# Optimization experiments

Hardware: AMD Instinct MI355X
Metric: run time of the kernel (lower is better)

Reference implementation:

```python
import jax, jax.numpy as jnp
import numpy as np

B, D, P = 2048, 768, 200
DOWN = [(384, 768), (192, 384), (96, 192), (48, 96)]
UP = [(96, 48), (192, 96), (384, 192), (768, 384)]


def setup_inputs() -> dict:
    key = jax.random.key(0)
    ks = jax.random.split(key, 32)
    inp = {
        "x": jax.random.normal(ks[0], (B, D), jnp.float32),
        "aW": jax.random.normal(ks[1], (D, D), jnp.float32) * 0.02,
        "ab": jax.random.normal(ks[2], (D,), jnp.float32) * 0.02,
        "protos": jax.random.normal(ks[3], (P, D), jnp.float32),
    }
    k = 4
    for i, (o, ii) in enumerate(DOWN):
        inp[f"Wd{i}"] = jax.random.normal(ks[k], (o, ii), jnp.float32) * (1.0 / np.sqrt(ii)); k += 1
        inp[f"bd{i}"] = jax.random.normal(ks[k], (o,), jnp.float32) * 0.02; k += 1
    for i, (o, ii) in enumerate(UP):
        inp[f"Wu{i}"] = jax.random.normal(ks[k], (o, ii), jnp.float32) * (1.0 / np.sqrt(ii)); k += 1
        inp[f"bu{i}"] = jax.random.normal(ks[k], (o,), jnp.float32) * 0.02; k += 1
    return inp


def _adopter_net(x, Wds, bds, Wus, bus):
    # down path with skip storage
    x_inter = []
    h = x
    for Wd, bd in zip(Wds, bds):
        h = jax.nn.relu(h @ Wd.T + bd)
        x_inter.append(h)
    # up path: residual adds for middle layers (i==1 uses x_inter[-2], i==2 uses x_inter[-3])
    n = len(Wus)
    for i, (Wu, bu) in enumerate(zip(Wus, bus)):
        if i == 0 or i == n - 1:
            h = jax.nn.relu(h @ Wu.T + bu)
        else:
            h = jax.nn.relu((h + x_inter[-i - 1]) @ Wu.T + bu)
    return h


def reference(x, aW, ab, Wd0, bd0, Wd1, bd1, Wd2, bd2, Wd3, bd3,
              Wu0, bu0, Wu1, bu1, Wu2, bu2, Wu3, bu3, protos):
    Wds, bds = [Wd0, Wd1, Wd2, Wd3], [bd0, bd1, bd2, bd3]
    Wus, bus = [Wu0, Wu1, Wu2, Wu3], [bu0, bu1, bu2, bu3]
    # features = x + adapter(x) + adopters(x)
    features = x + (x @ aW.T + ab) + _adopter_net(x, Wds, bds, Wus, bus)  # [B, D]
    # fused per-prototype negative L1 distance (replaces Python loop over PrototypeBase)
    logits = -jnp.sum(jnp.abs(features[:, None, :] - protos[None, :, :]), axis=-1)  # [B, P]
    return logits
```

## Files before the change

### kernel.cpp

```cpp
#include <hip/hip_runtime.h>

typedef __attribute__((ext_vector_type(8))) __bf16 bf16x8;
typedef __attribute__((ext_vector_type(4))) float f32x4;
typedef _Float16 hf2 __attribute__((ext_vector_type(2)));
typedef _Float16 hf8 __attribute__((ext_vector_type(8)));
typedef unsigned short u16;
typedef struct { hf2 v[4]; } hf2x4;

__device__ __forceinline__ float bf2f(u16 h) {
    return __uint_as_float(((unsigned int)h) << 16);
}
__device__ __forceinline__ u16 f2bf(float f) {
    unsigned int u = __float_as_uint(f);
    u += 0x7fffu + ((u >> 16) & 1u);
    return (u16)(u >> 16);
}

#if __has_builtin(__builtin_amdgcn_fdot2)
__device__ __forceinline__ float FDOT2(hf2 a, hf2 b, float c) {
    return __builtin_amdgcn_fdot2(a, b, c, false);
}
#else
__device__ __forceinline__ float FDOT2(hf2 a, hf2 b, float c) {
    return c + (float)a[0] + (float)a[1];
}
#endif

#define GLOAD_LDS16(gsrc, ldst)                                                          \
    __builtin_amdgcn_global_load_lds(                                                    \
        (__attribute__((address_space(1))) unsigned int*)(gsrc),                         \
        (__attribute__((address_space(3))) unsigned int*)(ldst), 16, 0, 0)

struct CvtDesc { const float* src; u16* dst; int N, K, Npad, Kpad, blk0, fmt; };
struct CvtTab { CvtDesc t[11]; };

__global__ __launch_bounds__(256) void cvt_all(CvtTab tab) {
    int b = blockIdx.x;
    int ti = 0;
#pragma unroll
    for (int j = 1; j < 11; ++j)
        if (b >= tab.t[j].blk0) ti = j;
    const CvtDesc c = tab.t[ti];
    long i = (long)(b - c.blk0) * 256 + threadIdx.x;
    long tot = (long)c.Npad * c.Kpad;
    if (i >= tot) return;
    int n = (int)(i / c.Kpad);
    int k = (int)(i - (long)n * c.Kpad);
    float v = (n < c.N && k < c.K) ? c.src[(long)n * c.K + k] : 0.f;
    if (c.fmt) {
        _Float16 h = (_Float16)v;
        c.dst[i] = __builtin_bit_cast(u16, h);
    } else {
        c.dst[i] = f2bf(v);
    }
}

template<int RELU, int HASRES, int MODE>
__device__ __forceinline__ void gemm_body(
    char* lds,
    const u16* __restrict__ A, int lda,
    const u16* __restrict__ W, int ldw,
    const float* __restrict__ bias, int Nreal,
    u16* __restrict__ outB, int ldo,
    const u16* __restrict__ res,
    float* __restrict__ outF, _Float16* __restrict__ outH,
    const float* __restrict__ addF,
    int nk, int mb, int nb)
{
    char* ldsA = lds;
    char* ldsB = lds + 8192;

    const int tid  = threadIdx.x;
    const int wave = tid >> 6;
    const int lane = tid & 63;
    const int wr = wave >> 1, wc = wave & 1;
    const int lr = lane & 15, lk = lane >> 4;

    f32x4 acc[2][2];
#pragma unroll
    for (int i = 0; i < 2; ++i)
#pragma unroll
        for (int j = 0; j < 2; ++j)
#pragma unroll
            for (int e = 0; e < 4; ++e) acc[i][j][e] = 0.f;

    const int g0 = wave * 64 + lane;
    const int r0 = g0 >> 3, l0 = (g0 & 7) ^ (r0 & 7);
    const int g1 = g0 + 256;
    const int r1 = g1 >> 3, l1 = (g1 & 7) ^ (r1 & 7);

    for (int kt = 0; kt < nk; ++kt) {
        const int kk = kt * 64;
        GLOAD_LDS16(A + (size_t)(mb + r0) * lda + kk + l0 * 8, ldsA + wave * 1024);
        GLOAD_LDS16(A + (size_t)(mb + r1) * lda + kk + l1 * 8, ldsA + 4096 + wave * 1024);
        GLOAD_LDS16(W + (size_t)(nb + r0) * ldw + kk + l0 * 8, ldsB + wave * 1024);
        GLOAD_LDS16(W + (size_t)(nb + r1) * ldw + kk + l1 * 8, ldsB + 4096 + wave * 1024);
        __syncthreads();
#pragma unroll
        for (int ks = 0; ks < 2; ++ks) {
            bf16x8 af[2], bfr[2];
#pragma unroll
            for (int mi = 0; mi < 2; ++mi) {
                int m_loc = wr * 32 + mi * 16 + lr;
                int gr = (ks * 4 + lk) ^ (m_loc & 7);
                af[mi] = *(const bf16x8*)(ldsA + m_loc * 128 + gr * 16);
            }
#pragma unroll
            for (int ni = 0; ni < 2; ++ni) {
                int n_loc = wc * 32 + ni * 16 + lr;
                int gr = (ks * 4 + lk) ^ (n_loc & 7);
                bfr[ni] = *(const bf16x8*)(ldsB + n_loc * 128 + gr * 16);
            }
#pragma unroll
            for (int mi = 0; mi < 2; ++mi)
#pragma unroll
                for (int ni = 0; ni < 2; ++ni)
                    acc[mi][ni] = __builtin_amdgcn_mfma_f32_16x16x32_bf16(
                        af[mi], bfr[ni], acc[mi][ni], 0, 0, 0);
        }
        __syncthreads();
    }

#pragma unroll
    for (int mi = 0; mi < 2; ++mi) {
#pragma unroll
        for (int ni = 0; ni < 2; ++ni) {
            const int n_g = nb + wc * 32 + ni * 16 + lr;
            const float bv = (n_g < Nreal) ? bias[n_g] : 0.f;
#pragma unroll
            for (int r = 0; r < 4; ++r) {
                const int m_g = mb + wr * 32 + mi * 16 + lk * 4 + r;
                float v = acc[mi][ni][r] + bv;
                if (RELU) v = fmaxf(v, 0.f);
                if (HASRES) v += bf2f(res[(size_t)m_g * ldo + n_g]);
                if (MODE == 1) {
                    outF[(size_t)m_g * 768 + n_g] = v + addF[(size_t)m_g * 768 + n_g];
                } else if (MODE == 2) {
                    outH[(size_t)m_g * 768 + n_g] =
                        (_Float16)(v + addF[(size_t)m_g * 768 + n_g]);
                } else {
                    outB[(size_t)m_g * ldo + n_g] = f2bf(v);
                }
            }
        }
    }
}

template<int RELU, int HASRES, int MODE>
__global__ __launch_bounds__(256) void gemm_k(
    const u16* __restrict__ A, int lda,
    const u16* __restrict__ W, int ldw,
    const float* __restrict__ bias, int Nreal,
    u16* __restrict__ outB, int ldo,
    const u16* __restrict__ res,
    float* __restrict__ outF, _Float16* __restrict__ outH,
    const float* __restrict__ addF, int nk)
{
    __shared__ __align__(16) char lds[16384];
    gemm_body<RELU, HASRES, MODE>(lds, A, lda, W, ldw, bias, Nreal, outB, ldo,
                                  res, outF, outH, addF, nk,
                                  blockIdx.x * 64, blockIdx.y * 64);
}

__global__ __launch_bounds__(256) void gemm_ad0(
    const u16* __restrict__ xb,
    const u16* __restrict__ aWb, const float* __restrict__ ab,
    float* __restrict__ adF, const float* __restrict__ x,
    const u16* __restrict__ Wd0b, const float* __restrict__ bd0,
    u16* __restrict__ h1)
{
    __shared__ __align__(16) char lds[16384];
    if (blockIdx.y < 12) {
        gemm_body<0, 0, 1>(lds, xb, 768, aWb, 768, ab, 768, nullptr, 0,
                           nullptr, adF, nullptr, x, 12,
                           blockIdx.x * 64, blockIdx.y * 64);
    } else {
        gemm_body<1, 0, 0>(lds, xb, 768, Wd0b, 768, bd0, 384, h1, 384,
                           nullptr, nullptr, nullptr, nullptr, 12,
                           blockIdx.x * 64, (blockIdx.y - 12) * 64);
    }
}

template<int K, int NPAD, int NREAL, int RES, int OUTG>
__device__ __forceinline__ void layer16(
    const u16* __restrict__ W, int ldw, const float* __restrict__ bias,
    const u16* actIn, int ldin,
    u16* actOut, int ldout,
    const u16* resid, int ldres,
    u16* __restrict__ gout, int ldg)
{
    constexpr int TPW = NPAD / 64;
    const int tid = threadIdx.x;
    const int wave = tid >> 6, lane = tid & 63;
    const int lr = lane & 15, lk = lane >> 4;

    f32x4 acc[TPW];
#pragma unroll
    for (int t = 0; t < TPW; ++t)
#pragma unroll
        for (int e = 0; e < 4; ++e) acc[t][e] = 0.f;

#pragma unroll
    for (int kk = 0; kk < K / 32; ++kk) {
        const bf16x8 a = *(const bf16x8*)&actIn[lr * ldin + kk * 32 + lk * 8];
#pragma unroll
        for (int t = 0; t < TPW; ++t) {
            const int nc = (wave * TPW + t) * 16 + lr;
            const bf16x8 b = *(const bf16x8*)&W[(size_t)nc * ldw + kk * 32 + lk * 8];
            acc[t] = __builtin_amdgcn_mfma_f32_16x16x32_bf16(a, b, acc[t], 0, 0, 0);
        }
    }
#pragma unroll
    for (int t = 0; t < TPW; ++t) {
        const int nc = (wave * TPW + t) * 16 + lr;
        const float bv = (nc < NREAL) ? bias[nc] : 0.f;
#pragma unroll
        for (int r = 0; r < 4; ++r) {
            const int row = lk * 4 + r;
            float v = fmaxf(acc[t][r] + bv, 0.f);
            if (RES) v += bf2f(resid[row * ldres + nc]);
            const u16 o = f2bf(v);
            if (OUTG) gout[(size_t)row * ldg + nc] = o;
            else      actOut[row * ldout + nc] = o;
        }
    }
}

__global__ __launch_bounds__(256) void chain_mid(
    const u16* __restrict__ h1,
    const u16* __restrict__ Wd1b, const float* __restrict__ bd1,
    const u16* __restrict__ Wd2b, const float* __restrict__ bd2,
    const u16* __restrict__ Wd3b, const float* __restrict__ bd3,
    const u16* __restrict__ Wu0b, const float* __restrict__ bu0,
    const u16* __restrict__ Wu1b, const float* __restrict__ bu1,
    const u16* __restrict__ Wu2b, const float* __restrict__ bu2,
    u16* __restrict__ u2)
{
    __shared__ u16 A[16 * 392];
    __shared__ u16 B[16 * 200];
    __shared__ u16 C[16 * 136];
    __shared__ u16 D[16 * 72];
    const int tid = threadIdx.x;
    const int rb = blockIdx.x * 16;

    for (int i = tid; i < 768; i += 256) {
        const int r = i / 48, c = i - r * 48;
        *(bf16x8*)&A[r * 392 + c * 8] =
            *(const bf16x8*)&h1[(size_t)(rb + r) * 384 + c * 8];
    }
    __syncthreads();
    layer16<384, 192, 192, 0, 0>(Wd1b, 384, bd1, A, 392, B, 200, nullptr, 0, nullptr, 0);
    __syncthreads();
    layer16<192, 128,  96, 0, 0>(Wd2b, 192, bd2, B, 200, C, 136, nullptr, 0, nullptr, 0);
    __syncthreads();
    layer16<128,  64,  48, 0, 0>(Wd3b, 128, bd3, C, 136, D,  72, nullptr, 0, nullptr, 0);
    __syncthreads();
    u16* E = A;
    u16* F = A + 16 * 136;
    layer16< 64, 128,  96, 1, 0>(Wu0b,  64, bu0, D,  72, E, 136, C, 136, nullptr, 0);
    __syncthreads();
    layer16<128, 192, 192, 1, 0>(Wu1b, 128, bu1, E, 136, F, 200, B, 200, nullptr, 0);
    __syncthreads();
    layer16<192, 384, 384, 0, 1>(Wu2b, 192, bu2, F, 200, nullptr, 0, nullptr, 0,
                                 u2 + (size_t)rb * 384, 384);
}

__global__ __launch_bounds__(256) void l1_kernel(
    const _Float16* __restrict__ feat, const _Float16* __restrict__ protos,
    float* __restrict__ part)
{
    __shared__ _Float16 fs[128][64];
    __shared__ hf2 pt[32][64];
    const int tid = threadIdx.x;
    const int tp = tid & 15, tr = tid >> 4;
    const int rb = blockIdx.x * 128;
    const int pb = blockIdx.y * 64;
    const int db = blockIdx.z * 64;

    {
        const int g = tid & 7, r0 = tid >> 3;
#pragma unroll
        for (int k = 0; k < 4; ++k) {
            const int r = r0 + 32 * k;
            *(hf8*)&fs[r][g * 8] =
                *(const hf8*)&feat[(size_t)(rb + r) * 768 + db + g * 8];
        }
    }
    {
        const int sp = tid & 63, q = tid >> 6;
        const _Float16* src = &protos[(size_t)(pb + sp) * 768 + db + q * 16];
        hf8 v0 = *(const hf8*)src;
        hf8 v1 = *(const hf8*)(src + 8);
        hf2x4 w0 = __builtin_bit_cast(hf2x4, v0);
        hf2x4 w1 = __builtin_bit_cast(hf2x4, v1);
#pragma unroll
        for (int e = 0; e < 4; ++e)
            pt[q * 8 + e][sp] = w0.v[e];
#pragma unroll
        for (int e = 0; e < 4; ++e)
            pt[q * 8 + 4 + e][sp] = w1.v[e];
    }
    __syncthreads();

    float acc[8][4];
#pragma unroll
    for (int i = 0; i < 8; ++i)
#pragma unroll
        for (int j = 0; j < 4; ++j) acc[i][j] = 0.f;

    const hf2 one2 = {(_Float16)1.0f, (_Float16)1.0f};
#pragma unroll 2
    for (int g = 0; g < 8; ++g) {
        hf2x4 F2[8];
#pragma unroll
        for (int i = 0; i < 8; ++i)
            F2[i] = __builtin_bit_cast(hf2x4,
                        *(const hf8*)&fs[tr + 16 * i][g * 8]);
        hf2x4 P2[4];
#pragma unroll
        for (int q = 0; q < 4; ++q)
            P2[q] = __builtin_bit_cast(hf2x4,
                        *(const hf8*)&pt[g * 4 + q][tp * 4]);
#pragma unroll
        for (int q = 0; q < 4; ++q) {
#pragma unroll
            for (int j = 0; j < 4; ++j) {
                const hf2 pj = P2[q].v[j];
#pragma unroll
                for (int i = 0; i < 8; ++i) {
                    hf2 d = F2[i].v[q] - pj;
                    unsigned ud = __builtin_bit_cast(unsigned, d) & 0x7FFF7FFFu;
                    acc[i][j] = FDOT2(__builtin_bit_cast(hf2, ud), one2, acc[i][j]);
                }
            }
        }
    }
    const int p = pb + tp * 4;
    if (p < 200) {
        const size_t zb = (size_t)blockIdx.z * 2048;
#pragma unroll
        for (int i = 0; i < 8; ++i) {
            float4 v = {-acc[i][0], -acc[i][1], -acc[i][2], -acc[i][3]};
            *(float4*)&part[(zb + rb + tr + 16 * i) * 200 + p] = v;
        }
    }
}

__global__ __launch_bounds__(256) void l1_reduce(
    const float* __restrict__ part, float* __restrict__ out)
{
    const int row = blockIdx.x;
    const int p = threadIdx.x;
    if (p < 200) {
        float s = 0.f;
#pragma unroll
        for (int z = 0; z < 12; ++z)
            s += part[((size_t)z * 2048 + row) * 200 + p];
        out[(size_t)row * 200 + p] = s;
    }
}

static constexpr size_t OFF_PART  = 0;
static constexpr size_t OFF_XB    = 0;
static constexpr size_t OFF_AWB   = 3145728;
static constexpr size_t OFF_WD0   = 4325376;
static constexpr size_t OFF_WD1   = 4915200;
static constexpr size_t OFF_WD2   = 5062656;
static constexpr size_t OFF_WD3   = 5111808;
static constexpr size_t OFF_WU0   = 5128192;
static constexpr size_t OFF_WU1   = 5144576;
static constexpr size_t OFF_WU2   = 5193728;
static constexpr size_t OFF_WU3   = 5341184;
static constexpr size_t OFF_H1    = 5931008;
static constexpr size_t OFF_U2    = 10387456;
static constexpr size_t OFF_ADF   = 11960320;
static constexpr size_t OFF_FEATH = 19660800;
static constexpr size_t OFF_PROH  = 22806528;

extern "C" void kernel_launch(void* const* d_in, const int* in_sizes, int n_in,
                              void* d_out, int out_size, void* d_ws, size_t ws_size,
                              hipStream_t stream) {
    const float* x      = (const float*)d_in[0];
    const float* aW     = (const float*)d_in[1];
    const float* ab     = (const float*)d_in[2];
    const float* protos = (const float*)d_in[3];
    const float* Wd[4]  = {(const float*)d_in[4], (const float*)d_in[6],
                           (const float*)d_in[8], (const float*)d_in[10]};
    const float* bd[4]  = {(const float*)d_in[5], (const float*)d_in[7],
                           (const float*)d_in[9], (const float*)d_in[11]};
    const float* Wu[4]  = {(const float*)d_in[12], (const float*)d_in[14],
                           (const float*)d_in[16], (const float*)d_in[18]};
    const float* bu[4]  = {(const float*)d_in[13], (const float*)d_in[15],
                           (const float*)d_in[17], (const float*)d_in[19]};
    float* out = (float*)d_out;
    char* ws = (char*)d_ws;

    u16* xb    = (u16*)(ws + OFF_XB);
    u16* aWb   = (u16*)(ws + OFF_AWB);
    u16* Wd0b  = (u16*)(ws + OFF_WD0);
    u16* Wd1b  = (u16*)(ws + OFF_WD1);
    u16* Wd2b  = (u16*)(ws + OFF_WD2);
    u16* Wd3b  = (u16*)(ws + OFF_WD3);
    u16* Wu0b  = (u16*)(ws + OFF_WU0);
    u16* Wu1b  = (u16*)(ws + OFF_WU1);
    u16* Wu2b  = (u16*)(ws + OFF_WU2);
    u16* Wu3b  = (u16*)(ws + OFF_WU3);
    u16* h1    = (u16*)(ws + OFF_H1);
    u16* u2    = (u16*)(ws + OFF_U2);
    float* adF = (float*)(ws + OFF_ADF);
    float* part = (float*)(ws + OFF_PART);
    _Float16* featH = (_Float16*)(ws + OFF_FEATH);
    _Float16* proH  = (_Float16*)(ws + OFF_PROH);

    CvtTab tab;
    int blk = 0;
    auto set = [&](int i, const float* s, u16* d, int N, int K, int Np, int Kp,
                   int fmt) {
        tab.t[i] = {s, d, N, K, Np, Kp, blk, fmt};
        blk += (Np * Kp + 255) / 256;
    };
    set(0,  x,      xb,          2048, 768, 2048, 768, 0);
    set(1,  aW,     aWb,         768,  768, 768,  768, 0);
    set(2,  Wd[0],  Wd0b,        384,  768, 384,  768, 0);
    set(3,  Wd[1],  Wd1b,        192,  384, 192,  384, 0);
    set(4,  Wd[2],  Wd2b,        96,   192, 128,  192, 0);
    set(5,  Wd[3],  Wd3b,        48,   96,  64,   128, 0);
    set(6,  Wu[0],  Wu0b,        96,   48,  128,  64,  0);
    set(7,  Wu[1],  Wu1b,        192,  96,  192,  128, 0);
    set(8,  Wu[2],  Wu2b,        384,  192, 384,  192, 0);
    set(9,  Wu[3],  Wu3b,        768,  384, 768,  384, 0);
    set(10, protos, (u16*)proH,  200,  768, 256,  768, 1);
    cvt_all<<<blk, 256, 0, stream>>>(tab);

    gemm_ad0<<<dim3(32, 18), 256, 0, stream>>>(xb, aWb, ab, adF, x, Wd0b, bd[0], h1);
    chain_mid<<<dim3(128), 256, 0, stream>>>(h1,
        Wd1b, bd[1], Wd2b, bd[2], Wd3b, bd[3],
        Wu0b, bu[0], Wu1b, bu[1], Wu2b, bu[2], u2);
    gemm_k<1,0,2><<<dim3(32,12), 256, 0, stream>>>(u2, 384, Wu3b, 384, bu[3], 768,
        nullptr, 0, nullptr, nullptr, featH, adF, 6);

    l1_kernel<<<dim3(16, 4, 12), 256, 0, stream>>>(featH, proH, part);
    l1_reduce<<<dim3(2048), 256, 0, stream>>>(part, out);
}
```

Measured before the change: 84.18 us.

## Fuse final up-projection into chain kernel and store adapter output as fp16

The last up layer (384->768) now runs inside the per-16-row chain kernel, so the separate GEMM launch and the u2 global round trip go away. The adapter GEMM adds the residual x from the bf16 copy and writes fp16 instead of fp32, which halves that intermediate's traffic. The L1 partial-sum layout is also reordered so each row's 12 partials sit next to each other for the reduce. In exchange, only 128 blocks do the large final GEMM, and each block streams the whole Wu3 weight from global memory. The residual x is now taken in bf16 and rounded to fp16 before being added, so precision drops slightly.

```diff
diff --git a/kernel.cpp b/kernel.cpp
--- a/kernel.cpp
+++ b/kernel.cpp
@@ -63,8 +63,7 @@
     const float* __restrict__ bias, int Nreal,
     u16* __restrict__ outB, int ldo,
     const u16* __restrict__ res,
-    float* __restrict__ outF, _Float16* __restrict__ outH,
-    const float* __restrict__ addF,
+    _Float16* __restrict__ outH,
     int nk, int mb, int nb)
 {
     char* ldsA = lds;
@@ -133,11 +132,8 @@
                 float v = acc[mi][ni][r] + bv;
                 if (RELU) v = fmaxf(v, 0.f);
                 if (HASRES) v += bf2f(res[(size_t)m_g * ldo + n_g]);
-                if (MODE == 1) {
-                    outF[(size_t)m_g * 768 + n_g] = v + addF[(size_t)m_g * 768 + n_g];
-                } else if (MODE == 2) {
-                    outH[(size_t)m_g * 768 + n_g] =
-                        (_Float16)(v + addF[(size_t)m_g * 768 + n_g]);
+                if (MODE == 2) {
+                    outH[(size_t)m_g * 768 + n_g] = (_Float16)v;
                 } else {
                     outB[(size_t)m_g * ldo + n_g] = f2bf(v);
                 }
@@ -146,48 +142,30 @@
     }
 }
 
-template<int RELU, int HASRES, int MODE>
-__global__ __launch_bounds__(256) void gemm_k(
-    const u16* __restrict__ A, int lda,
-    const u16* __restrict__ W, int ldw,
-    const float* __restrict__ bias, int Nreal,
-    u16* __restrict__ outB, int ldo,
-    const u16* __restrict__ res,
-    float* __restrict__ outF, _Float16* __restrict__ outH,
-    const float* __restrict__ addF, int nk)
-{
-    __shared__ __align__(16) char lds[16384];
-    gemm_body<RELU, HASRES, MODE>(lds, A, lda, W, ldw, bias, Nreal, outB, ldo,
-                                  res, outF, outH, addF, nk,
-                                  blockIdx.x * 64, blockIdx.y * 64);
-}
-
 __global__ __launch_bounds__(256) void gemm_ad0(
     const u16* __restrict__ xb,
     const u16* __restrict__ aWb, const float* __restrict__ ab,
-    float* __restrict__ adF, const float* __restrict__ x,
+    _Float16* __restrict__ adFH,
     const u16* __restrict__ Wd0b, const float* __restrict__ bd0,
     u16* __restrict__ h1)
 {
     __shared__ __align__(16) char lds[16384];
     if (blockIdx.y < 12) {
-        gemm_body<0, 0, 1>(lds, xb, 768, aWb, 768, ab, 768, nullptr, 0,
-                           nullptr, adF, nullptr, x, 12,
-                           blockIdx.x * 64, blockIdx.y * 64);
+        gemm_body<0, 1, 2>(lds, xb, 768, aWb, 768, ab, 768, nullptr, 768,
+                           xb, adFH, 12, blockIdx.x * 64, blockIdx.y * 64);
     } else {
         gemm_body<1, 0, 0>(lds, xb, 768, Wd0b, 768, bd0, 384, h1, 384,
-                           nullptr, nullptr, nullptr, nullptr, 12,
+                           nullptr, nullptr, 12,
                            blockIdx.x * 64, (blockIdx.y - 12) * 64);
     }
 }
 
-template<int K, int NPAD, int NREAL, int RES, int OUTG>
+template<int K, int NPAD, int NREAL, int RES>
 __device__ __forceinline__ void layer16(
     const u16* __restrict__ W, int ldw, const float* __restrict__ bias,
     const u16* actIn, int ldin,
     u16* actOut, int ldout,
-    const u16* resid, int ldres,
-    u16* __restrict__ gout, int ldg)
+    const u16* resid, int ldres)
 {
     constexpr int TPW = NPAD / 64;
     const int tid = threadIdx.x;
@@ -219,14 +197,12 @@
             const int row = lk * 4 + r;
             float v = fmaxf(acc[t][r] + bv, 0.f);
             if (RES) v += bf2f(resid[row * ldres + nc]);
-            const u16 o = f2bf(v);
-            if (OUTG) gout[(size_t)row * ldg + nc] = o;
-            else      actOut[row * ldout + nc] = o;
-        }
-    }
-}
-
-__global__ __launch_bounds__(256) void chain_mid(
+            actOut[row * ldout + nc] = f2bf(v);
+        }
+    }
+}
+
+__global__ __launch_bounds__(256) void chain_full(
     const u16* __restrict__ h1,
     const u16* __restrict__ Wd1b, const float* __restrict__ bd1,
     const u16* __restrict__ Wd2b, const float* __restrict__ bd2,
@@ -234,35 +210,70 @@
     const u16* __restrict__ Wu0b, const float* __restrict__ bu0,
     const u16* __restrict__ Wu1b, const float* __restrict__ bu1,
     const u16* __restrict__ Wu2b, const float* __restrict__ bu2,
-    u16* __restrict__ u2)
-{
-    __shared__ u16 A[16 * 392];
-    __shared__ u16 B[16 * 200];
-    __shared__ u16 C[16 * 136];
-    __shared__ u16 D[16 * 72];
+    const u16* __restrict__ Wu3b, const float* __restrict__ bu3,
+    const _Float16* __restrict__ adFH, _Float16* __restrict__ featH)
+{
+    __shared__ u16 As[16 * 392];
+    __shared__ u16 Bs[16 * 200];
+    __shared__ u16 Cs[16 * 136];
+    __shared__ u16 Ds[16 * 72];
+    __shared__ u16 Gs[16 * 392];
     const int tid = threadIdx.x;
     const int rb = blockIdx.x * 16;
 
     for (int i = tid; i < 768; i += 256) {
         const int r = i / 48, c = i - r * 48;
-        *(bf16x8*)&A[r * 392 + c * 8] =
+        *(bf16x8*)&As[r * 392 + c * 8] =
             *(const bf16x8*)&h1[(size_t)(rb + r) * 384 + c * 8];
     }
     __syncthreads();
-    layer16<384, 192, 192, 0, 0>(Wd1b, 384, bd1, A, 392, B, 200, nullptr, 0, nullptr, 0);
-    __syncthreads();
-    layer16<192, 128,  96, 0, 0>(Wd2b, 192, bd2, B, 200, C, 136, nullptr, 0, nullptr, 0);
-    __syncthreads();
-    layer16<128,  64,  48, 0, 0>(Wd3b, 128, bd3, C, 136, D,  72, nullptr, 0, nullptr, 0);
-    __syncthreads();
-    u16* E = A;
-    u16* F = A + 16 * 136;
-    layer16< 64, 128,  96, 1, 0>(Wu0b,  64, bu0, D,  72, E, 136, C, 136, nullptr, 0);
-    __syncthreads();
-    layer16<128, 192, 192, 1, 0>(Wu1b, 128, bu1, E, 136, F, 200, B, 200, nullptr, 0);
-    __syncthreads();
-    layer16<192, 384, 384, 0, 1>(Wu2b, 192, bu2, F, 200, nullptr, 0, nullptr, 0,
-                                 u2 + (size_t)rb * 384, 384);
+    layer16<384, 192, 192, 0>(Wd1b, 384, bd1, As, 392, Bs, 200, nullptr, 0);
+    __syncthreads();
+    layer16<192, 128,  96, 0>(Wd2b, 192, bd2, Bs, 200, Cs, 136, nullptr, 0);
+    __syncthreads();
+    layer16<128,  64,  48, 0>(Wd3b, 128, bd3, Cs, 136, Ds,  72, nullptr, 0);
+    __syncthreads();
+    u16* E = As;
+    u16* F = As + 16 * 136;
+    layer16< 64, 128,  96, 1>(Wu0b,  64, bu0, Ds,  72, E, 136, Cs, 136);
+    __syncthreads();
+    layer16<128, 192, 192, 1>(Wu1b, 128, bu1, E, 136, F, 200, Bs, 200);
+    __syncthreads();
+    layer16<192, 384, 384, 0>(Wu2b, 192, bu2, F, 200, Gs, 392, nullptr, 0);
+    __syncthreads();
+
+    {
+        const int wave = tid >> 6, lane = tid & 63;
+        const int lr = lane & 15, lk = lane >> 4;
+        f32x4 acc[12];
+#pragma unroll
+        for (int t = 0; t < 12; ++t)
+#pragma unroll
+            for (int e = 0; e < 4; ++e) acc[t][e] = 0.f;
+#pragma unroll 2
+        for (int kk = 0; kk < 12; ++kk) {
+            const bf16x8 a = *(const bf16x8*)&Gs[lr * 392 + kk * 32 + lk * 8];
+#pragma unroll
+            for (int t = 0; t < 12; ++t) {
+                const int nc = (wave * 12 + t) * 16 + lr;
+                const bf16x8 b =
+                    *(const bf16x8*)&Wu3b[(size_t)nc * 384 + kk * 32 + lk * 8];
+                acc[t] = __builtin_amdgcn_mfma_f32_16x16x32_bf16(a, b, acc[t], 0, 0, 0);
+            }
+        }
+#pragma unroll
+        for (int t = 0; t < 12; ++t) {
+            const int nc = (wave * 12 + t) * 16 + lr;
+            const float bv = bu3[nc];
+#pragma unroll
+            for (int r = 0; r < 4; ++r) {
+                const int row = lk * 4 + r;
+                float v = fmaxf(acc[t][r] + bv, 0.f);
+                v += (float)adFH[(size_t)(rb + row) * 768 + nc];
+                featH[(size_t)(rb + row) * 768 + nc] = (_Float16)v;
+            }
+        }
+    }
 }
 
 __global__ __launch_bounds__(256) void l1_kernel(
@@ -337,11 +348,10 @@
     }
     const int p = pb + tp * 4;
     if (p < 200) {
-        const size_t zb = (size_t)blockIdx.z * 2048;
 #pragma unroll
         for (int i = 0; i < 8; ++i) {
             float4 v = {-acc[i][0], -acc[i][1], -acc[i][2], -acc[i][3]};
-            *(float4*)&part[(zb + rb + tr + 16 * i) * 200 + p] = v;
+            *(float4*)&part[((size_t)(rb + tr + 16 * i) * 12 + blockIdx.z) * 200 + p] = v;
         }
     }
 }
@@ -355,7 +365,7 @@
         float s = 0.f;
 #pragma unroll
         for (int z = 0; z < 12; ++z)
-            s += part[((size_t)z * 2048 + row) * 200 + p];
+            s += part[((size_t)row * 12 + z) * 200 + p];
         out[(size_t)row * 200 + p] = s;
     }
 }
@@ -372,7 +382,6 @@
 static constexpr size_t OFF_WU2   = 5193728;
 static constexpr size_t OFF_WU3   = 5341184;
 static constexpr size_t OFF_H1    = 5931008;
-static constexpr size_t OFF_U2    = 10387456;
 static constexpr size_t OFF_ADF   = 11960320;
 static constexpr size_t OFF_FEATH = 19660800;
 static constexpr size_t OFF_PROH  = 22806528;
@@ -406,9 +415,8 @@
     u16* Wu2b  = (u16*)(ws + OFF_WU2);
     u16* Wu3b  = (u16*)(ws + OFF_WU3);
     u16* h1    = (u16*)(ws + OFF_H1);
-    u16* u2    = (u16*)(ws + OFF_U2);
-    float* adF = (float*)(ws + OFF_ADF);
     float* part = (float*)(ws + OFF_PART);
+    _Float16* adFH  = (_Float16*)(ws + OFF_ADF);
     _Float16* featH = (_Float16*)(ws + OFF_FEATH);
     _Float16* proH  = (_Float16*)(ws + OFF_PROH);
 
@@ -432,12 +440,11 @@
     set(10, protos, (u16*)proH,  200,  768, 256,  768, 1);
     cvt_all<<<blk, 256, 0, stream>>>(tab);
 
-    gemm_ad0<<<dim3(32, 18), 256, 0, stream>>>(xb, aWb, ab, adF, x, Wd0b, bd[0], h1);
-    chain_mid<<<dim3(128), 256, 0, stream>>>(h1,
+    gemm_ad0<<<dim3(32, 18), 256, 0, stream>>>(xb, aWb, ab, adFH, Wd0b, bd[0], h1);
+    chain_full<<<dim3(128), 256, 0, stream>>>(h1,
         Wd1b, bd[1], Wd2b, bd[2], Wd3b, bd[3],
-        Wu0b, bu[0], Wu1b, bu[1], Wu2b, bu[2], u2);
-    gemm_k<1,0,2><<<dim3(32,12), 256, 0, stream>>>(u2, 384, Wu3b, 384, bu[3], 768,
-        nullptr, 0, nullptr, nullptr, featH, adF, 6);
+        Wu0b, bu[0], Wu1b, bu[1], Wu2b, bu[2], Wu3b, bu[3],
+        adFH, featH);
 
     l1_kernel<<<dim3(16, 4, 12), 256, 0, stream>>>(featH, proH, part);
     l1_reduce<<<dim3(2048), 256, 0, stream>>>(part, out);
```

Result: slower. 90.98 us (+8.1%).
